# Performance work log

Hardware: AMD Instinct MI355X
Metric: run time of the kernel (lower is better)

The kernel has to match this reference:

```python
import jax, jax.numpy as jnp
import numpy as np

BATCH_SIZE = 2
EMBEDDING_DIM = 128
NUM_HEADS = 8
HEAD_DIM = EMBEDDING_DIM // NUM_HEADS  # 16
SEQ_LEN = 2048


def _split_heads(x, B, S):
    # Faithful to torch: reshape (B,S,head_dim,H) then transpose(2,3),(1,2)
    # -> (B,H,S,head_dim); head index is the fastest-varying dim of embedding.
    return x.reshape(B, S, HEAD_DIM, NUM_HEADS).transpose(0, 3, 1, 2)


def setup_inputs() -> dict:
    key = jax.random.key(0)
    k0, k1, k2, k3, k4 = jax.random.split(key, 5)
    inp = {
        "input_embeddings": jax.random.normal(k0, (BATCH_SIZE, SEQ_LEN, EMBEDDING_DIM), dtype=jnp.float32),
        "token_attention_masks_source": jax.random.randint(k1, (BATCH_SIZE, SEQ_LEN), 0, 2, dtype=jnp.int32),
        "token_attention_masks_target": jnp.ones((BATCH_SIZE, SEQ_LEN), dtype=jnp.int32),
        "masked": 0,  # encoder self-attention path (masked == False)
        # params: torch.rand -> uniform [0,1)
        "w_query": jax.random.uniform(k2, (EMBEDDING_DIM, EMBEDDING_DIM), dtype=jnp.float32),
        "w_key": jax.random.uniform(k3, (EMBEDDING_DIM, EMBEDDING_DIM), dtype=jnp.float32),
        "w_value": jax.random.uniform(k4, (EMBEDDING_DIM, EMBEDDING_DIM), dtype=jnp.float32),
    }
    return inp


def reference(input_embeddings, token_attention_masks_source, token_attention_masks_target, masked, w_query, w_key, w_value):
    B = BATCH_SIZE
    if not masked:
        S = token_attention_masks_source.shape[1]
    else:
        S = token_attention_masks_target.shape[1]

    # encoder_output_embedding is None in this path -> query from input_embeddings
    q = _split_heads(input_embeddings @ w_query, B, S)  # (B,H,S,hd)
    k = _split_heads(input_embeddings @ w_key, B, S)
    v = _split_heads(input_embeddings @ w_value, B, S)

    scale = jnp.einsum('bhqd,bhkd->bhqk', q, k) / jnp.sqrt(jnp.float32(HEAD_DIM))

    if not masked:
        # additive key mask: 0 -> -1000, 1 -> 0; broadcast over query dim
        add_mask = jnp.where(token_attention_masks_source == 0, jnp.float32(-1000.0), jnp.float32(0.0))
        scores = scale + add_mask[:, None, None, :]
    else:
        scores = scale

    probs = jax.nn.softmax(scores, axis=-1)
    ctx = jnp.einsum('bhqk,bhkd->bhqd', probs, v)  # (B,H,S,hd)
    # inverse of the split: (B,H,S,hd) -> (B,S,hd,H) -> (B,S,E)
    out = ctx.transpose(0, 2, 3, 1).reshape(B, S, HEAD_DIM * NUM_HEADS)
    return out
```

## Files before the change

### kernel.cpp

```cpp
#include <hip/hip_runtime.h>
#include <hip/hip_bf16.h>

#define B 2
#define S 2048
#define E 128
#define H 8
#define HD 16
#define BH (B*H)

#define RPB 4
#define KT 64

typedef __attribute__((ext_vector_type(8))) short bf16x8;
typedef __attribute__((ext_vector_type(4))) float f32x4;

__device__ __forceinline__ unsigned short f2b(float f) {
    const unsigned u = __float_as_uint(f);
    return (unsigned short)((u + 0x7FFFu + ((u >> 16) & 1u)) >> 16);
}
__device__ __forceinline__ float b2f(unsigned short u) {
    return __uint_as_float((unsigned)u << 16);
}

__global__ __launch_bounds__(64) void prep(
    const int* __restrict__ mask, const int* __restrict__ masked_p,
    int* __restrict__ pos, int* __restrict__ cnt,
    unsigned short* __restrict__ Kxg, unsigned short* __restrict__ Btg)
{
    const int bh = blockIdx.x;
    const int b = bh >> 3, h = bh & 7;
    const int lane = threadIdx.x;
    const int masked = *masked_p;

    int v[32];
    #pragma unroll
    for (int c = 0; c < 32; ++c)
        v[c] = mask[b * S + c * 64 + lane];

    int base = 0;
    #pragma unroll
    for (int c = 0; c < 32; ++c) {
        const bool keep = (masked != 0) || (v[c] != 0);
        const unsigned long long bal = __ballot(keep);
        if (h == 0) {
            const int my = base + (int)__popcll(bal & ((1ULL << lane) - 1ULL));
            pos[b * S + c * 64 + lane] = keep ? my : -1;
        }
        base += (int)__popcll(bal);
    }
    int cn = base;
    if (cn == 0) {
        if (h == 0) {
            #pragma unroll
            for (int c = 0; c < 32; ++c)
                pos[b * S + c * 64 + lane] = c * 64 + lane;
        }
        cn = S;
    }
    if (h == 0 && lane == 0) cnt[b] = cn;

    const int pad = ((cn + KT - 1) / KT) * KT;
    const int nrows = pad - cn;
    unsigned short* KxB = Kxg + (size_t)bh * S * 32;
    unsigned short* BtB = Btg + (size_t)bh * S * 32;
    for (int idx = lane; idx < nrows * 16; idx += 64) {
        const int row = cn + (idx >> 4), d = idx & 15;
        KxB[row * 32 + d]      = 0;
        KxB[row * 32 + 16 + d] = 0;
        BtB[((row >> 4) * 16 + d) * 32 + (row & 15) * 2]     = 0;
        BtB[((row >> 4) * 16 + d) * 32 + (row & 15) * 2 + 1] = 0;
    }
}

__global__ __launch_bounds__(384) void qkv_proj(
    const float* __restrict__ x,
    const float* __restrict__ wq,
    const float* __restrict__ wk,
    const float* __restrict__ wv,
    const int* __restrict__ pos,
    float* __restrict__ Q,
    unsigned short* __restrict__ Kxg, unsigned short* __restrict__ Btg)
{
    __shared__ float xs[RPB][E];
    const int row0 = blockIdx.x * RPB;
    const int tid  = threadIdx.x;
    const int mat  = tid >> 7;
    const int c    = tid & 127;

    for (int idx = tid; idx < RPB * E; idx += 384)
        ((float*)xs)[idx] = x[(size_t)row0 * E + idx];
    __syncthreads();

    const float* w = (mat == 0) ? wq : (mat == 1) ? wk : wv;
    float a[RPB];
    #pragma unroll
    for (int rr = 0; rr < RPB; ++rr) a[rr] = 0.f;

    for (int i = 0; i < E; ++i) {
        const float wv_ = w[i * E + c];
        #pragma unroll
        for (int rr = 0; rr < RPB; ++rr)
            a[rr] = fmaf(xs[rr][i], wv_, a[rr]);
    }

    const int h = c & 7, d = c >> 3;
    if (mat == 0) {
        #pragma unroll
        for (int rr = 0; rr < RPB; ++rr) {
            const int row = row0 + rr;
            const int b = row >> 11, s = row & 2047;
            Q[(((size_t)(b * H + h)) * S + s) * HD + d] = a[rr] * 0.25f;
        }
    } else if (mat == 1) {
        #pragma unroll
        for (int rr = 0; rr < RPB; ++rr) {
            const int row = row0 + rr;
            const int p_ = pos[row];
            if (p_ >= 0) {
                const int b = row >> 11;
                const unsigned short kh = f2b(a[rr]);
                const unsigned short kl = f2b(a[rr] - b2f(kh));
                unsigned short* kx = Kxg + (size_t)(b * H + h) * S * 32
                                   + (size_t)p_ * 32;
                kx[d]      = kh;
                kx[16 + d] = kl;
            }
        }
    } else {
        #pragma unroll
        for (int rr = 0; rr < RPB; ++rr) {
            const int row = row0 + rr;
            const int p_ = pos[row];
            if (p_ >= 0) {
                const int b = row >> 11;
                const unsigned short vh = f2b(a[rr]);
                const unsigned short vl = f2b(a[rr] - b2f(vh));
                unsigned short* bt = Btg + (size_t)(b * H + h) * S * 32
                                   + ((size_t)(p_ >> 4) * 16 + d) * 32
                                   + (p_ & 15) * 2;
                *(unsigned*)bt = (unsigned)vh | ((unsigned)vl << 16);
            }
        }
    }
}

__global__ __launch_bounds__(128, 4) void attn(
    const float* __restrict__ Q,
    const unsigned short* __restrict__ Kxg,
    const unsigned short* __restrict__ Btg,
    const int* __restrict__ cnt,
    float* __restrict__ out)
{
    const int bh    = blockIdx.y;
    const int b     = bh >> 3;
    const int h     = bh & 7;
    const int qtile = blockIdx.x;
    const int tid   = threadIdx.x;
    const int wid   = tid >> 6;
    const int lane  = tid & 63;
    const int col   = lane & 15;
    const int g     = lane >> 4;
    const int qrow0 = qtile * 32 + wid * 16;
    const int cn    = cnt[b];
    const int nt    = (cn + KT - 1) >> 6;

    const unsigned short* KxB = Kxg + (size_t)bh * S * 32;
    const unsigned short* BtB = Btg + (size_t)bh * S * 32;

    bf16x8 qh, ql;
    {
        const float* qp = Q + ((size_t)bh * S + qrow0 + col) * HD + 8 * (g & 1);
        #pragma unroll
        for (int i = 0; i < 8; ++i) {
            const float f = qp[i];
            const unsigned short hi = f2b(f);
            qh[i] = (short)hi;
            ql[i] = (short)f2b(f - b2f(hi));
        }
    }

    float m = -1e30f, l = 0.f;
    f32x4 acc = {0.f, 0.f, 0.f, 0.f};

#define LOADT(KA, VB, TBASE)                                              \
    {                                                                     \
        const int base_ = (TBASE);                                        \
        _Pragma("unroll")                                                 \
        for (int kb = 0; kb < 4; ++kb) {                                  \
            KA[kb] = *(const bf16x8*)(                                    \
                KxB + (size_t)(base_ + kb * 16 + col) * 32 + 8 * g);      \
            VB[kb] = *(const bf16x8*)(                                    \
                BtB + (size_t)((base_ >> 4) + kb) * 512 + col * 32 + 8 * g); \
        }                                                                 \
    }

#define COMPUTE(KA, VB, TBASE)                                            \
    {                                                                     \
        const int base_ = (TBASE);                                        \
        f32x4 sc[4];                                                      \
        _Pragma("unroll")                                                 \
        for (int kb = 0; kb < 4; ++kb) {                                  \
            f32x4 c_ = {0.f, 0.f, 0.f, 0.f};                              \
            c_ = __builtin_amdgcn_mfma_f32_16x16x32_bf16(KA[kb], qh, c_, 0, 0, 0); \
            c_ = __builtin_amdgcn_mfma_f32_16x16x32_bf16(KA[kb], ql, c_, 0, 0, 0); \
            sc[kb] = c_;                                                  \
        }                                                                 \
        if (base_ + KT > cn) {                                            \
            _Pragma("unroll")                                             \
            for (int kb = 0; kb < 4; ++kb)                                \
                _Pragma("unroll")                                         \
                for (int r = 0; r < 4; ++r)                               \
                    if (base_ + kb * 16 + 4 * g + r >= cn) sc[kb][r] = -1e30f; \
        }                                                                 \
        float tm = sc[0][0];                                              \
        _Pragma("unroll")                                                 \
        for (int kb = 0; kb < 4; ++kb)                                    \
            _Pragma("unroll")                                             \
            for (int r = 0; r < 4; ++r) tm = fmaxf(tm, sc[kb][r]);        \
        tm = fmaxf(tm, __shfl_xor(tm, 16));                               \
        tm = fmaxf(tm, __shfl_xor(tm, 32));                               \
        if (__any(tm > m)) {                                              \
            const float mn = fmaxf(m, tm);                                \
            const float alpha = __expf(m - mn);                           \
            m = mn;                                                       \
            l *= alpha;                                                   \
            _Pragma("unroll")                                             \
            for (int r = 0; r < 4; ++r)                                   \
                acc[r] *= __shfl(alpha, 4 * g + r);                       \
        }                                                                 \
        _Pragma("unroll")                                                 \
        for (int kb = 0; kb < 4; ++kb) {                                  \
            const float p0 = __expf(sc[kb][0] - m);                       \
            const float p1 = __expf(sc[kb][1] - m);                       \
            const float p2 = __expf(sc[kb][2] - m);                       \
            const float p3 = __expf(sc[kb][3] - m);                       \
            l += (p0 + p1) + (p2 + p3);                                   \
            union { unsigned u[4]; bf16x8 v; } pa;                        \
            const unsigned b0 = (unsigned)f2b(p0);                        \
            const unsigned b1 = (unsigned)f2b(p1);                        \
            const unsigned b2 = (unsigned)f2b(p2);                        \
            const unsigned b3 = (unsigned)f2b(p3);                        \
            pa.u[0] = b0 | (b0 << 16);                                    \
            pa.u[1] = b1 | (b1 << 16);                                    \
            pa.u[2] = b2 | (b2 << 16);                                    \
            pa.u[3] = b3 | (b3 << 16);                                    \
            acc = __builtin_amdgcn_mfma_f32_16x16x32_bf16(pa.v, VB[kb], acc, 0, 0, 0); \
        }                                                                 \
    }

    bf16x8 kaA[4], vbA[4], kaB[4], vbB[4];
    LOADT(kaA, vbA, 0);
    for (int kt = 0; kt < nt; kt += 2) {
        if (kt + 1 < nt) LOADT(kaB, vbB, (kt + 1) * KT);
        COMPUTE(kaA, vbA, kt * KT);
        if (kt + 1 < nt) {
            if (kt + 2 < nt) LOADT(kaA, vbA, (kt + 2) * KT);
            COMPUTE(kaB, vbB, (kt + 1) * KT);
        }
    }
#undef LOADT
#undef COMPUTE

    l += __shfl_xor(l, 16);
    l += __shfl_xor(l, 32);

    const float inv = 1.f / l;
    #pragma unroll
    for (int r = 0; r < 4; ++r) {
        const float ir = __shfl(inv, 4 * g + r);
        out[((size_t)(b * S + qrow0 + 4 * g + r)) * E + col * 8 + h] = acc[r] * ir;
    }
}

extern "C" void kernel_launch(void* const* d_in, const int* in_sizes, int n_in,
                              void* d_out, int out_size, void* d_ws, size_t ws_size,
                              hipStream_t stream) {
    int ix = 0, im0 = -1, isc = -1, iw[3] = {-1, -1, -1}, nw = 0;
    for (int i = 0; i < n_in; ++i) {
        const int sz = in_sizes[i];
        if (sz == B * S * E) ix = i;
        else if (sz == B * S) { if (im0 < 0) im0 = i; }
        else if (sz == E * E) { if (nw < 3) iw[nw++] = i; }
        else if (sz == 1 && isc < 0) isc = i;
    }
    if (im0 < 0) im0 = 1;
    if (isc < 0) isc = 3;
    if (nw < 3) { iw[0] = n_in - 3; iw[1] = n_in - 2; iw[2] = n_in - 1; }

    const float* x        = (const float*)d_in[ix];
    const int*   src_mask = (const int*)d_in[im0];
    const int*   masked_p = (const int*)d_in[isc];
    const float* wq       = (const float*)d_in[iw[0]];
    const float* wk       = (const float*)d_in[iw[1]];
    const float* wv       = (const float*)d_in[iw[2]];
    float*       out      = (float*)d_out;

    float*          Qw  = (float*)d_ws;
    unsigned short* Kxg = (unsigned short*)(Qw + (size_t)BH * S * HD);
    unsigned short* Btg = Kxg + (size_t)BH * S * 32;
    int*            pos = (int*)(Btg + (size_t)BH * S * 32);
    int*            cnt = pos + B * S;

    prep<<<BH, 64, 0, stream>>>(src_mask, masked_p, pos, cnt, Kxg, Btg);
    qkv_proj<<<B * S / RPB, 384, 0, stream>>>(x, wq, wk, wv, pos, Qw, Kxg, Btg);
    attn<<<dim3(S / 32, BH), 128, 0, stream>>>(Qw, Kxg, Btg, cnt, out);
}
```

Before: 47.25 us.

## Remove prep kernel by recomputing mask compaction inside projection and attention

Drops the separate prep launch that computed compacted key positions, counts and zeroed padding rows. Each qkv_proj block now recomputes the prefix-sum ballot over the batch mask for its rows, and each attention block recounts the kept keys. The padded V entries are zeroed in registers while loading instead of in memory. This saves one kernel launch and a dependency at the cost of redundant mask scans in every block. The K padding rows are no longer zeroed and rely on existing score masking.

Measured after the change: 57.85 us. +22.4%, slower.

```diff
diff --git a/kernel.cpp b/kernel.cpp
--- a/kernel.cpp
+++ b/kernel.cpp
@@ -22,73 +22,47 @@
     return __uint_as_float((unsigned)u << 16);
 }
 
-__global__ __launch_bounds__(64) void prep(
-    const int* __restrict__ mask, const int* __restrict__ masked_p,
-    int* __restrict__ pos, int* __restrict__ cnt,
-    unsigned short* __restrict__ Kxg, unsigned short* __restrict__ Btg)
-{
-    const int bh = blockIdx.x;
-    const int b = bh >> 3, h = bh & 7;
-    const int lane = threadIdx.x;
-    const int masked = *masked_p;
-
-    int v[32];
-    #pragma unroll
-    for (int c = 0; c < 32; ++c)
-        v[c] = mask[b * S + c * 64 + lane];
-
-    int base = 0;
-    #pragma unroll
-    for (int c = 0; c < 32; ++c) {
-        const bool keep = (masked != 0) || (v[c] != 0);
-        const unsigned long long bal = __ballot(keep);
-        if (h == 0) {
-            const int my = base + (int)__popcll(bal & ((1ULL << lane) - 1ULL));
-            pos[b * S + c * 64 + lane] = keep ? my : -1;
-        }
-        base += (int)__popcll(bal);
-    }
-    int cn = base;
-    if (cn == 0) {
-        if (h == 0) {
-            #pragma unroll
-            for (int c = 0; c < 32; ++c)
-                pos[b * S + c * 64 + lane] = c * 64 + lane;
-        }
-        cn = S;
-    }
-    if (h == 0 && lane == 0) cnt[b] = cn;
-
-    const int pad = ((cn + KT - 1) / KT) * KT;
-    const int nrows = pad - cn;
-    unsigned short* KxB = Kxg + (size_t)bh * S * 32;
-    unsigned short* BtB = Btg + (size_t)bh * S * 32;
-    for (int idx = lane; idx < nrows * 16; idx += 64) {
-        const int row = cn + (idx >> 4), d = idx & 15;
-        KxB[row * 32 + d]      = 0;
-        KxB[row * 32 + 16 + d] = 0;
-        BtB[((row >> 4) * 16 + d) * 32 + (row & 15) * 2]     = 0;
-        BtB[((row >> 4) * 16 + d) * 32 + (row & 15) * 2 + 1] = 0;
-    }
-}
-
 __global__ __launch_bounds__(384) void qkv_proj(
     const float* __restrict__ x,
     const float* __restrict__ wq,
     const float* __restrict__ wk,
     const float* __restrict__ wv,
-    const int* __restrict__ pos,
+    const int* __restrict__ mask,
+    const int* __restrict__ masked_p,
     float* __restrict__ Q,
     unsigned short* __restrict__ Kxg, unsigned short* __restrict__ Btg)
 {
     __shared__ float xs[RPB][E];
     const int row0 = blockIdx.x * RPB;
+    const int b    = row0 >> 11;
     const int tid  = threadIdx.x;
+    const int lane = tid & 63;
     const int mat  = tid >> 7;
     const int c    = tid & 127;
 
     for (int idx = tid; idx < RPB * E; idx += 384)
         ((float*)xs)[idx] = x[(size_t)row0 * E + idx];
+
+    const int masked = *masked_p;
+    const int tchunk = (row0 & 2047) >> 6;
+    int base = 0, myval = -1;
+    for (int it = 0; it < 32; ++it) {
+        const bool keep = (masked != 0) || (mask[b * S + it * 64 + lane] != 0);
+        const unsigned long long bal = __ballot(keep);
+        if (it == tchunk)
+            myval = keep ? base + (int)__popcll(bal & ((1ULL << lane) - 1ULL))
+                         : -1;
+        base += (int)__popcll(bal);
+    }
+    int posr[RPB];
+    #pragma unroll
+    for (int rr = 0; rr < RPB; ++rr)
+        posr[rr] = __shfl(myval, (row0 + rr) & 63);
+    if (base == 0) {
+        #pragma unroll
+        for (int rr = 0; rr < RPB; ++rr)
+            posr[rr] = (row0 & 2047) + rr;
+    }
     __syncthreads();
 
     const float* w = (mat == 0) ? wq : (mat == 1) ? wk : wv;
@@ -107,17 +81,14 @@
     if (mat == 0) {
         #pragma unroll
         for (int rr = 0; rr < RPB; ++rr) {
-            const int row = row0 + rr;
-            const int b = row >> 11, s = row & 2047;
+            const int s = (row0 & 2047) + rr;
             Q[(((size_t)(b * H + h)) * S + s) * HD + d] = a[rr] * 0.25f;
         }
     } else if (mat == 1) {
         #pragma unroll
         for (int rr = 0; rr < RPB; ++rr) {
-            const int row = row0 + rr;
-            const int p_ = pos[row];
+            const int p_ = posr[rr];
             if (p_ >= 0) {
-                const int b = row >> 11;
                 const unsigned short kh = f2b(a[rr]);
                 const unsigned short kl = f2b(a[rr] - b2f(kh));
                 unsigned short* kx = Kxg + (size_t)(b * H + h) * S * 32
@@ -129,10 +100,8 @@
     } else {
         #pragma unroll
         for (int rr = 0; rr < RPB; ++rr) {
-            const int row = row0 + rr;
-            const int p_ = pos[row];
+            const int p_ = posr[rr];
             if (p_ >= 0) {
-                const int b = row >> 11;
                 const unsigned short vh = f2b(a[rr]);
                 const unsigned short vl = f2b(a[rr] - b2f(vh));
                 unsigned short* bt = Btg + (size_t)(b * H + h) * S * 32
@@ -148,7 +117,8 @@
     const float* __restrict__ Q,
     const unsigned short* __restrict__ Kxg,
     const unsigned short* __restrict__ Btg,
-    const int* __restrict__ cnt,
+    const int* __restrict__ mask,
+    const int* __restrict__ masked_p,
     float* __restrict__ out)
 {
     const int bh    = blockIdx.y;
@@ -161,8 +131,18 @@
     const int col   = lane & 15;
     const int g     = lane >> 4;
     const int qrow0 = qtile * 32 + wid * 16;
-    const int cn    = cnt[b];
-    const int nt    = (cn + KT - 1) >> 6;
+
+    int cn = 0;
+    {
+        const int masked = *masked_p;
+        for (int it = 0; it < 32; ++it) {
+            const bool keep = (masked != 0) ||
+                              (mask[b * S + it * 64 + lane] != 0);
+            cn += (int)__popcll(__ballot(keep));
+        }
+        if (cn == 0) cn = S;
+    }
+    const int nt = (cn + KT - 1) >> 6;
 
     const unsigned short* KxB = Kxg + (size_t)bh * S * 32;
     const unsigned short* BtB = Btg + (size_t)bh * S * 32;
@@ -191,6 +171,14 @@
                 KxB + (size_t)(base_ + kb * 16 + col) * 32 + 8 * g);      \
             VB[kb] = *(const bf16x8*)(                                    \
                 BtB + (size_t)((base_ >> 4) + kb) * 512 + col * 32 + 8 * g); \
+        }                                                                 \
+        if (base_ + KT > cn) {                 \
+            _Pragma("unroll")                                             \
+            for (int kb = 0; kb < 4; ++kb)                                \
+                _Pragma("unroll")                                         \
+                for (int i = 0; i < 8; ++i)                               \
+                    if (base_ + kb * 16 + 4 * g + (i >> 1) >= cn)         \
+                        VB[kb][i] = 0;                                    \
         }                                                                 \
     }
 
@@ -298,10 +286,9 @@
     float*          Qw  = (float*)d_ws;
     unsigned short* Kxg = (unsigned short*)(Qw + (size_t)BH * S * HD);
     unsigned short* Btg = Kxg + (size_t)BH * S * 32;
-    int*            pos = (int*)(Btg + (size_t)BH * S * 32);
-    int*            cnt = pos + B * S;
-
-    prep<<<BH, 64, 0, stream>>>(src_mask, masked_p, pos, cnt, Kxg, Btg);
-    qkv_proj<<<B * S / RPB, 384, 0, stream>>>(x, wq, wk, wv, pos, Qw, Kxg, Btg);
-    attn<<<dim3(S / 32, BH), 128, 0, stream>>>(Qw, Kxg, Btg, cnt, out);
-}
+
+    qkv_proj<<<B * S / RPB, 384, 0, stream>>>(
+        x, wq, wk, wv, src_mask, masked_p, Qw, Kxg, Btg);
+    attn<<<dim3(S / 32, BH), 128, 0, stream>>>(
+        Qw, Kxg, Btg, src_mask, masked_p, out);
+}
```

## Stage K/V tiles in double-buffered LDS shared by four waves per block

Applied to the files above, without the earlier changes.

The attention kernel now uses 256-thread blocks covering 64 query rows. Each K and V tile is loaded cooperatively into padded, double-buffered shared memory, and every wave reads its MFMA operands from there instead of from global memory. This cuts redundant global/L2 traffic, since four waves now share each tile instead of two. The cost is a block-wide barrier per tile, extra LDS reads and half as many blocks in the grid.

Result: no change. 47.03 us (-0.5%).

```diff
diff --git a/kernel.cpp b/kernel.cpp
--- a/kernel.cpp
+++ b/kernel.cpp
@@ -10,6 +10,7 @@
 
 #define RPB 4
 #define KT 64
+#define LP 40
 
 typedef __attribute__((ext_vector_type(8))) short bf16x8;
 typedef __attribute__((ext_vector_type(4))) float f32x4;
@@ -144,13 +145,16 @@
     }
 }
 
-__global__ __launch_bounds__(128, 4) void attn(
+__global__ __launch_bounds__(256) void attn(
     const float* __restrict__ Q,
     const unsigned short* __restrict__ Kxg,
     const unsigned short* __restrict__ Btg,
     const int* __restrict__ cnt,
     float* __restrict__ out)
 {
+    __shared__ unsigned short Ks[2][KT * LP];
+    __shared__ unsigned short Bs[2][KT * LP];
+
     const int bh    = blockIdx.y;
     const int b     = bh >> 3;
     const int h     = bh & 7;
@@ -160,12 +164,17 @@
     const int lane  = tid & 63;
     const int col   = lane & 15;
     const int g     = lane >> 4;
-    const int qrow0 = qtile * 32 + wid * 16;
+    const int qrow0 = qtile * 64 + wid * 16;
     const int cn    = cnt[b];
     const int nt    = (cn + KT - 1) >> 6;
 
     const unsigned short* KxB = Kxg + (size_t)bh * S * 32;
     const unsigned short* BtB = Btg + (size_t)bh * S * 32;
+
+    const int srow = tid >> 2;
+    const int sc4  = tid & 3;
+    const int soff = srow * 32 + sc4 * 8;
+    const int doff = srow * LP + sc4 * 8;
 
     bf16x8 qh, ql;
     {
@@ -182,27 +191,16 @@
     float m = -1e30f, l = 0.f;
     f32x4 acc = {0.f, 0.f, 0.f, 0.f};
 
-#define LOADT(KA, VB, TBASE)                                              \
-    {                                                                     \
-        const int base_ = (TBASE);                                        \
-        _Pragma("unroll")                                                 \
-        for (int kb = 0; kb < 4; ++kb) {                                  \
-            KA[kb] = *(const bf16x8*)(                                    \
-                KxB + (size_t)(base_ + kb * 16 + col) * 32 + 8 * g);      \
-            VB[kb] = *(const bf16x8*)(                                    \
-                BtB + (size_t)((base_ >> 4) + kb) * 512 + col * 32 + 8 * g); \
-        }                                                                 \
-    }
-
-#define COMPUTE(KA, VB, TBASE)                                            \
+#define COMPUTE(BUF, TBASE)                                               \
     {                                                                     \
         const int base_ = (TBASE);                                        \
         f32x4 sc[4];                                                      \
         _Pragma("unroll")                                                 \
         for (int kb = 0; kb < 4; ++kb) {                                  \
+            const bf16x8 ka = *(const bf16x8*)&Ks[BUF][(kb * 16 + col) * LP + 8 * g]; \
             f32x4 c_ = {0.f, 0.f, 0.f, 0.f};                              \
-            c_ = __builtin_amdgcn_mfma_f32_16x16x32_bf16(KA[kb], qh, c_, 0, 0, 0); \
-            c_ = __builtin_amdgcn_mfma_f32_16x16x32_bf16(KA[kb], ql, c_, 0, 0, 0); \
+            c_ = __builtin_amdgcn_mfma_f32_16x16x32_bf16(ka, qh, c_, 0, 0, 0); \
+            c_ = __builtin_amdgcn_mfma_f32_16x16x32_bf16(ka, ql, c_, 0, 0, 0); \
             sc[kb] = c_;                                                  \
         }                                                                 \
         if (base_ + KT > cn) {                                            \
@@ -244,21 +242,35 @@
             pa.u[1] = b1 | (b1 << 16);                                    \
             pa.u[2] = b2 | (b2 << 16);                                    \
             pa.u[3] = b3 | (b3 << 16);                                    \
-            acc = __builtin_amdgcn_mfma_f32_16x16x32_bf16(pa.v, VB[kb], acc, 0, 0, 0); \
+            const bf16x8 vb = *(const bf16x8*)&Bs[BUF][(kb * 16 + col) * LP + 8 * g]; \
+            acc = __builtin_amdgcn_mfma_f32_16x16x32_bf16(pa.v, vb, acc, 0, 0, 0); \
         }                                                                 \
     }
 
-    bf16x8 kaA[4], vbA[4], kaB[4], vbB[4];
-    LOADT(kaA, vbA, 0);
-    for (int kt = 0; kt < nt; kt += 2) {
-        if (kt + 1 < nt) LOADT(kaB, vbB, (kt + 1) * KT);
-        COMPUTE(kaA, vbA, kt * KT);
-        if (kt + 1 < nt) {
-            if (kt + 2 < nt) LOADT(kaA, vbA, (kt + 2) * KT);
-            COMPUTE(kaB, vbB, (kt + 1) * KT);
-        }
-    }
-#undef LOADT
+    {
+        const bf16x8 k0 = *(const bf16x8*)(KxB + soff);
+        const bf16x8 v0 = *(const bf16x8*)(BtB + soff);
+        *(bf16x8*)&Ks[0][doff] = k0;
+        *(bf16x8*)&Bs[0][doff] = v0;
+    }
+    __syncthreads();
+
+    for (int kt = 0; kt < nt; ++kt) {
+        const int cur = kt & 1;
+        bf16x8 kN, vN;
+        const bool more = (kt + 1 < nt);
+        if (more) {
+            const size_t tb = (size_t)(kt + 1) * 2048 + soff;
+            kN = *(const bf16x8*)(KxB + tb);
+            vN = *(const bf16x8*)(BtB + tb);
+        }
+        COMPUTE(cur, kt * KT);
+        if (more) {
+            *(bf16x8*)&Ks[cur ^ 1][doff] = kN;
+            *(bf16x8*)&Bs[cur ^ 1][doff] = vN;
+        }
+        __syncthreads();
+    }
 #undef COMPUTE
 
     l += __shfl_xor(l, 16);
@@ -303,5 +315,5 @@
 
     prep<<<BH, 64, 0, stream>>>(src_mask, masked_p, pos, cnt, Kxg, Btg);
     qkv_proj<<<B * S / RPB, 384, 0, stream>>>(x, wq, wk, wv, pos, Qw, Kxg, Btg);
-    attn<<<dim3(S / 32, BH), 128, 0, stream>>>(Qw, Kxg, Btg, cnt, out);
-}
+    attn<<<dim3(S / 64, BH), 256, 0, stream>>>(Qw, Kxg, Btg, cnt, out);
+}
```
